# Optimization experiments

Measured on AMD Instinct MI355X. Metric: run time of the kernel, lower is better.

## Reference

```python
import jax, jax.numpy as jnp
import numpy as np

N_NODES, N_EDGES = 50000, 800000
IN_X, OUT_X = 32, 64
IN_EN, OUT_EN = 32, 64
HIDDEN = [64, 128, 32]  # build_mlp hidden sizes


def _mlp_params(key, dims):
    ps = []
    for i, (a, b) in enumerate(zip(dims[:-1], dims[1:])):
        k1, k2, key = jax.random.split(key, 3)
        s = 1.0 / np.sqrt(a)
        ps.append(jax.random.uniform(k1, (a, b), jnp.float32, -s, s))
        ps.append(jax.random.uniform(k2, (b,), jnp.float32, -s, s))
    return ps


def _mlp_apply(h, params):
    n_layers = len(params) // 2
    for i in range(n_layers):
        W, b = params[2 * i], params[2 * i + 1]
        h = h @ W + b
        if i < n_layers - 1:
            h = jax.nn.relu(h)
    return h


def setup_inputs() -> dict:
    key = jax.random.key(0)
    kx, ken, ks, kd, kt, kp, k_ten, k_pen = jax.random.split(key, 8)
    inp = {
        "x": jax.random.normal(kx, (N_NODES, IN_X), jnp.float32),
        "en": jax.random.normal(ken, (N_NODES, IN_EN), jnp.float32),
        "src": jax.random.randint(ks, (N_EDGES,), 0, N_NODES),
        "dst": jax.random.randint(kd, (N_EDGES,), 0, N_NODES),
    }
    # linear layers theta/phi for x
    kt1, kt2 = jax.random.split(kt)
    kp1, kp2 = jax.random.split(kp)
    s = 1.0 / np.sqrt(IN_X)
    inp["theta_W"] = jax.random.uniform(kt1, (IN_X, OUT_X), jnp.float32, -s, s)
    inp["theta_b"] = jax.random.uniform(kt2, (OUT_X,), jnp.float32, -s, s)
    inp["phi_W"] = jax.random.uniform(kp1, (IN_X, OUT_X), jnp.float32, -s, s)
    inp["phi_b"] = jax.random.uniform(kp2, (OUT_X,), jnp.float32, -s, s)
    # MLPs theta_en / phi_en: in_en -> 64 -> 128 -> 32 -> out_en
    dims = [IN_EN] + HIDDEN + [OUT_EN]
    for name, p in zip(
        ["ten_W0", "ten_b0", "ten_W1", "ten_b1", "ten_W2", "ten_b2", "ten_W3", "ten_b3"],
        _mlp_params(k_ten, dims)):
        inp[name] = p
    for name, p in zip(
        ["pen_W0", "pen_b0", "pen_W1", "pen_b1", "pen_W2", "pen_b2", "pen_W3", "pen_b3"],
        _mlp_params(k_pen, dims)):
        inp[name] = p
    return inp


def reference(x, en, src, dst,
              theta_W, theta_b, phi_W, phi_b,
              ten_W0, ten_b0, ten_W1, ten_b1, ten_W2, ten_b2, ten_W3, ten_b3,
              pen_W0, pen_b0, pen_W1, pen_b1, pen_W2, pen_b2, pen_W3, pen_b3):
    n = x.shape[0]
    ten = [ten_W0, ten_b0, ten_W1, ten_b1, ten_W2, ten_b2, ten_W3, ten_b3]
    pen = [pen_W0, pen_b0, pen_W1, pen_b1, pen_W2, pen_b2, pen_W3, pen_b3]

    # --- message: per-edge features ---
    dx = x[dst] - x[src]                       # [E, in_x]
    edge_x = dx @ theta_W + theta_b + (x @ phi_W + phi_b)[src]   # [E, out_x]
    den = en[dst] - en[src]                    # [E, in_en]
    edge_en = _mlp_apply(den, ten) + _mlp_apply(en, pen)[src]    # [E, out_en]

    # --- aggregate: max over incoming edge_x, mean over incoming edge_en ---
    deg = jax.ops.segment_sum(jnp.ones((src.shape[0],), x.dtype), dst, num_segments=n)
    has_in = (deg > 0)[:, None]
    x_new = jax.ops.segment_max(edge_x, dst, num_segments=n)
    x_new = jnp.where(has_in, x_new, 0.0)      # DGL zero-fills empty nodes
    en_sum = jax.ops.segment_sum(edge_en, dst, num_segments=n)
    en_new = en_sum / jnp.maximum(deg, 1.0)[:, None]

    # knn_graph rebuild is a library call (excluded from the kernel target);
    # return the updated node features carried by the new graph.
    return jnp.concatenate([x_new, en_new], axis=-1)  # [N, out_x + out_en]
```

## Files before the change

### kernel.cpp

```cpp
#include <hip/hip_runtime.h>

#define N_NODES 50000
#define N_EDGES 800000

typedef __attribute__((ext_vector_type(8))) short short8v;
typedef __attribute__((ext_vector_type(4))) float f32x4;

__device__ __forceinline__ ushort bf16hi(float v) {
  return (ushort)(__float_as_uint(v) >> 16);
}

__device__ __forceinline__ void split8(const float v[8], short8v& hh, short8v& ll) {
#pragma unroll
  for (int j = 0; j < 8; ++j) {
    unsigned uv = __float_as_uint(v[j]);
    hh[j] = (short)(uv >> 16);
    float hf = __uint_as_float(uv & 0xFFFF0000u);
    ll[j] = (short)(__float_as_uint(v[j] - hf) >> 16);
  }
}

#define C1_X 196
#define C1_CNT 3125
#define C1_PACK 120

constexpr int XK_THT = 0;
constexpr int XK_PHT = 2048;
constexpr int XK_THB = 4096;
constexpr int XK_PHB = 4160;
constexpr int XK_SZ  = 4224;

__global__ void __launch_bounds__(256) combo1_kernel(
    const float* __restrict__ x,
    const float* __restrict__ thW, const float* __restrict__ thB,
    const float* __restrict__ phW, const float* __restrict__ phB,
    float* __restrict__ out, float* __restrict__ gp,
    const int* __restrict__ dst, int* __restrict__ counts,
    const float* __restrict__ tW1, const float* __restrict__ tW2,
    const float* __restrict__ tW0, const float* __restrict__ pW0,
    const float* __restrict__ pW1, const float* __restrict__ pW2,
    const float* __restrict__ pW3, ushort* __restrict__ wp) {
  const int b = blockIdx.x;
  const int tid = threadIdx.x;
  if (b < C1_X) {
    __shared__ __align__(16) float sm[XK_SZ];
    for (int t = tid; t < 2048; t += 256) {
      int j = t >> 5, k = t & 31;
      sm[XK_THT + t] = thW[k * 64 + j];
      sm[XK_PHT + t] = phW[k * 64 + j];
    }
    for (int t = tid; t < 64; t += 256) {
      sm[XK_THB + t] = thB[t];
      sm[XK_PHB + t] = phB[t];
    }
    __syncthreads();
    int n = b * 256 + tid;
    if (n >= N_NODES) return;

    float xv[32];
    {
      const float4* p = (const float4*)(x + (long)n * 32);
#pragma unroll
      for (int q = 0; q < 8; ++q) {
        float4 v = p[q];
        xv[q * 4 + 0] = v.x; xv[q * 4 + 1] = v.y;
        xv[q * 4 + 2] = v.z; xv[q * 4 + 3] = v.w;
      }
    }
    float* ao = out + (long)n * 128;
    float* go = gp + (long)n * 128;
    for (int j = 0; j < 64; ++j) {
      float dth = 0.f, dph = 0.f;
#pragma unroll
      for (int k = 0; k < 32; ++k) {
        dth += xv[k] * sm[XK_THT + j * 32 + k];
        dph += xv[k] * sm[XK_PHT + j * 32 + k];
      }
      ao[j] = sm[XK_THB + j] + dth;
      go[j] = sm[XK_PHB + j] + dph - dth;
    }
  } else if (b < C1_X + C1_CNT) {
    int e = (b - C1_X) * 256 + tid;
    if (e < N_EDGES) atomicAdd(&counts[dst[e]], 1);
  } else {
    int t = (b - C1_X - C1_CNT) * 256 + tid;
    if (t >= 30720) return;
    float v;
    int hi_off, lo_off;
    if (t < 8192) {
      int fi = t >> 9, lane = (t >> 3) & 63, j = t & 7;
      int r = fi >> 1, f = fi & 1;
      int k2 = r * 16 + (lane & 15);
      int jg = f * 32 + (lane >> 4) * 8 + j;
      v = tW1[jg * 128 + k2];
      hi_off = t; lo_off = 8192 + t;
    } else if (t < 12288) {
      int t2 = t - 8192;
      int fi = t2 >> 9, lane = (t2 >> 3) & 63, j = t2 & 7;
      int tt = fi >> 2, f2 = fi & 3;
      int cc = tt * 16 + (lane & 15);
      int qq = (lane >> 4) & 3;
      int k2 = f2 * 32 + (j >> 2) * 16 + qq * 4 + (j & 3);
      v = tW2[k2 * 32 + cc];
      hi_off = 16384 + t2; lo_off = 20480 + t2;
    } else if (t < 16384) {
      int t3 = t - 12288;
      const float* M = (t3 < 2048) ? tW0 : pW0;
      int tt3 = t3 & 2047;
      int fi = tt3 >> 9, lane = (tt3 >> 3) & 63, j = tt3 & 7;
      int row = fi * 16 + (lane & 15);
      int k = (lane >> 4) * 8 + j;
      v = M[k * 64 + row];
      hi_off = ((t3 < 2048) ? 24576 : 28672) + tt3;
      lo_off = hi_off + 2048;
    } else if (t < 24576) {
      int t5 = t - 16384;
      int fi = t5 >> 9, lane = (t5 >> 3) & 63, j = t5 & 7;
      int r = fi >> 1, f = fi & 1;
      int row = r * 16 + (lane & 15);
      int sig = 32 * f + 16 * (j >> 2) + 4 * ((lane >> 4) & 3) + (j & 3);
      v = pW1[sig * 128 + row];
      hi_off = 32768 + t5; lo_off = 40960 + t5;
    } else if (t < 28672) {
      int t6 = t - 24576;
      int fi = t6 >> 9, lane = (t6 >> 3) & 63, j = t6 & 7;
      int tt = fi >> 2, f2 = fi & 3;
      int cc = tt * 16 + (lane & 15);
      int qq = (lane >> 4) & 3;
      int k2 = f2 * 32 + (j >> 2) * 16 + qq * 4 + (j & 3);
      v = pW2[k2 * 32 + cc];
      hi_off = 49152 + t6; lo_off = 53248 + t6;
    } else {
      int t7 = t - 28672;
      int fi = t7 >> 9, lane = (t7 >> 3) & 63, j = t7 & 7;
      int row = fi * 16 + (lane & 15);
      int sig = 16 * (j >> 2) + 4 * ((lane >> 4) & 3) + (j & 3);
      v = pW3[sig * 64 + row];
      hi_off = 57344 + t7; lo_off = 59392 + t7;
    }
    ushort h = bf16hi(v);
    float hf = __uint_as_float((unsigned)h << 16);
    ushort l = bf16hi(v - hf);
    wp[hi_off] = h;
    wp[lo_off] = l;
  }
}

#define SCAN_NB ((N_NODES + 1023) / 1024)

__global__ void __launch_bounds__(1024) scan1_kernel(
    const int* __restrict__ counts, int* __restrict__ offsets,
    int* __restrict__ bsum) {
  __shared__ int wsum[16];
  int t = threadIdx.x, b = blockIdx.x;
  int idx = b * 1024 + t;
  int c = (idx < N_NODES) ? counts[idx] : 0;
  int lane = t & 63, w = t >> 6;
  int v = c;
#pragma unroll
  for (int off = 1; off < 64; off <<= 1) {
    int tt = __shfl_up(v, off);
    if (lane >= off) v += tt;
  }
  if (lane == 63) wsum[w] = v;
  __syncthreads();
  int wpre = 0;
#pragma unroll
  for (int i = 0; i < 16; ++i) {
    int tt = wsum[i];
    if (i < w) wpre += tt;
  }
  int incl = v + wpre;
  if (idx < N_NODES) offsets[idx] = incl - c;
  if (t == 1023) bsum[b] = incl;
}

__global__ void __launch_bounds__(1024) scan2_kernel(
    const int* __restrict__ bsum, int* __restrict__ offsets,
    int* __restrict__ counts) {
  __shared__ int sb[SCAN_NB];
  int t = threadIdx.x, b = blockIdx.x;
  if (t < SCAN_NB) sb[t] = bsum[t];
  __syncthreads();
  int bpre = 0;
#pragma unroll
  for (int i = 0; i < SCAN_NB; ++i) {
    int tt = sb[i];
    if (i < b) bpre += tt;
  }
  int idx = b * 1024 + t;
  if (idx < N_NODES) {
    int v = offsets[idx] + bpre;
    offsets[idx] = v;
    counts[idx] = v;
  }
  if (b == 0 && t == 0) offsets[N_NODES] = N_EDGES;
}

#define C2_EN 391
#define C2_SC 1563

__global__ void __launch_bounds__(512) combo2_kernel(
    const float* __restrict__ en, const ushort* __restrict__ wp,
    const float* __restrict__ pb0, const float* __restrict__ pb1,
    const float* __restrict__ pb2, const float* __restrict__ pb3,
    float* __restrict__ u, float* __restrict__ gp,
    const int* __restrict__ src, const int* __restrict__ dst,
    int* __restrict__ cursor, int2* __restrict__ csr) {
  const int b = blockIdx.x;
  const int tid = threadIdx.x;
  if (b < C2_EN) {
    __shared__ __align__(16) ushort lds[36864];
    {
      const uint4* s4 = (const uint4*)(wp + 24576);
      uint4* d4 = (uint4*)lds;
      for (int i = tid; i < 4608; i += 512) d4[i] = s4[i];
    }
    __syncthreads();
    const int lane = tid & 63, q = lane >> 4, c = lane & 15, wv = tid >> 6;
    const int n = (b * 8 + wv) * 16 + c;
    const bool valid = n < N_NODES;

    float env[8];
#pragma unroll
    for (int j = 0; j < 8; ++j) env[j] = 0.f;
    if (valid) {
      const float4* p = (const float4*)(en + (long)n * 32 + q * 8);
      float4 e0 = p[0], e1 = p[1];
      env[0] = e0.x; env[1] = e0.y; env[2] = e0.z; env[3] = e0.w;
      env[4] = e1.x; env[5] = e1.y; env[6] = e1.z; env[7] = e1.w;
    }
    short8v beh, bel;
    split8(env, beh, bel);

    const short8v* TW0H = (const short8v*)(lds);
    const short8v* TW0L = (const short8v*)(lds + 2048);
    const short8v* PW0H = (const short8v*)(lds + 4096);
    const short8v* PW0L = (const short8v*)(lds + 6144);
    const short8v* NW1H = (const short8v*)(lds + 8192);
    const short8v* NW1L = (const short8v*)(lds + 16384);
    const short8v* NW2H = (const short8v*)(lds + 24576);
    const short8v* NW2L = (const short8v*)(lds + 28672);
    const short8v* NW3H = (const short8v*)(lds + 32768);
    const short8v* NW3L = (const short8v*)(lds + 34816);

#pragma unroll
    for (int t = 0; t < 4; ++t) {
      f32x4 a = {0.f, 0.f, 0.f, 0.f};
      short8v ah = TW0H[t * 64 + lane], al = TW0L[t * 64 + lane];
      a = __builtin_amdgcn_mfma_f32_16x16x32_bf16(ah, beh, a, 0, 0, 0);
      a = __builtin_amdgcn_mfma_f32_16x16x32_bf16(al, beh, a, 0, 0, 0);
      a = __builtin_amdgcn_mfma_f32_16x16x32_bf16(ah, bel, a, 0, 0, 0);
      if (valid) *(f32x4*)(u + (long)n * 64 + t * 16 + q * 4) = a;
    }

    float h0v[4][4];
#pragma unroll
    for (int t = 0; t < 4; ++t) {
      f32x4 a = *(const f32x4*)(pb0 + t * 16 + q * 4);
      short8v ah = PW0H[t * 64 + lane], al = PW0L[t * 64 + lane];
      a = __builtin_amdgcn_mfma_f32_16x16x32_bf16(ah, beh, a, 0, 0, 0);
      a = __builtin_amdgcn_mfma_f32_16x16x32_bf16(al, beh, a, 0, 0, 0);
      a = __builtin_amdgcn_mfma_f32_16x16x32_bf16(ah, bel, a, 0, 0, 0);
#pragma unroll
      for (int g = 0; g < 4; ++g) h0v[t][g] = fmaxf(a[g], 0.f);
    }

    short8v b1h[2], b1l[2];
#pragma unroll
    for (int f = 0; f < 2; ++f) {
      float tmp[8];
#pragma unroll
      for (int j = 0; j < 8; ++j) tmp[j] = h0v[2 * f + (j >> 2)][j & 3];
      split8(tmp, b1h[f], b1l[f]);
    }

    float h1v[8][4];
#pragma unroll
    for (int r = 0; r < 8; ++r) {
      f32x4 a = *(const f32x4*)(pb1 + r * 16 + q * 4);
#pragma unroll
      for (int f = 0; f < 2; ++f) {
        short8v ah = NW1H[(r * 2 + f) * 64 + lane];
        short8v al = NW1L[(r * 2 + f) * 64 + lane];
        a = __builtin_amdgcn_mfma_f32_16x16x32_bf16(ah, b1h[f], a, 0, 0, 0);
        a = __builtin_amdgcn_mfma_f32_16x16x32_bf16(al, b1h[f], a, 0, 0, 0);
        a = __builtin_amdgcn_mfma_f32_16x16x32_bf16(ah, b1l[f], a, 0, 0, 0);
      }
#pragma unroll
      for (int g = 0; g < 4; ++g) h1v[r][g] = fmaxf(a[g], 0.f);
    }

    short8v b2h[4], b2l[4];
#pragma unroll
    for (int f2 = 0; f2 < 4; ++f2) {
      float tmp[8];
#pragma unroll
      for (int j = 0; j < 8; ++j) tmp[j] = h1v[2 * f2 + (j >> 2)][j & 3];
      split8(tmp, b2h[f2], b2l[f2]);
    }

    float h2v[2][4];
#pragma unroll
    for (int tt = 0; tt < 2; ++tt) {
      f32x4 a = *(const f32x4*)(pb2 + tt * 16 + q * 4);
#pragma unroll
      for (int f2 = 0; f2 < 4; ++f2) {
        short8v ah = NW2H[(tt * 4 + f2) * 64 + lane];
        short8v al = NW2L[(tt * 4 + f2) * 64 + lane];
        a = __builtin_amdgcn_mfma_f32_16x16x32_bf16(ah, b2h[f2], a, 0, 0, 0);
        a = __builtin_amdgcn_mfma_f32_16x16x32_bf16(al, b2h[f2], a, 0, 0, 0);
        a = __builtin_amdgcn_mfma_f32_16x16x32_bf16(ah, b2l[f2], a, 0, 0, 0);
      }
#pragma unroll
      for (int g = 0; g < 4; ++g) h2v[tt][g] = fmaxf(a[g], 0.f);
    }

    short8v b3h, b3l;
    {
      float tmp[8];
#pragma unroll
      for (int j = 0; j < 8; ++j) tmp[j] = h2v[j >> 2][j & 3];
      split8(tmp, b3h, b3l);
    }

#pragma unroll
    for (int t = 0; t < 4; ++t) {
      f32x4 a = *(const f32x4*)(pb3 + t * 16 + q * 4);
      short8v ah = NW3H[t * 64 + lane], al = NW3L[t * 64 + lane];
      a = __builtin_amdgcn_mfma_f32_16x16x32_bf16(ah, b3h, a, 0, 0, 0);
      a = __builtin_amdgcn_mfma_f32_16x16x32_bf16(al, b3h, a, 0, 0, 0);
      a = __builtin_amdgcn_mfma_f32_16x16x32_bf16(ah, b3l, a, 0, 0, 0);
      if (valid) *(f32x4*)(gp + (long)n * 128 + 64 + t * 16 + q * 4) = a;
    }
  } else {
    int e = (b - C2_EN) * 512 + tid;
    if (e >= N_EDGES) return;
    int d = dst[e];
    int slot = atomicAdd(&cursor[d], 1);
    csr[slot] = make_int2(src[e], d);
  }
}

__global__ void __launch_bounds__(512) mlp_edge_kernel(
    const float* __restrict__ u,
    const int2* __restrict__ csr,
    const float* __restrict__ b0g, const float* __restrict__ b1g,
    const float* __restrict__ b2g,
    const ushort* __restrict__ wp,
    float* __restrict__ h2sum) {
  __shared__ __align__(16) ushort lds[24576];
  {
    const uint4* s4 = (const uint4*)wp;
    uint4* d4 = (uint4*)lds;
    for (int i = threadIdx.x; i < 3072; i += 512) d4[i] = s4[i];
  }
  __syncthreads();

  const int orig = blockIdx.x;
  const int xcd = orig & 7, loc = orig >> 3;
  const int blk = (xcd < 2) ? xcd * 782 + loc
                            : 2 * 782 + (xcd - 2) * 781 + loc;

  const int lane = threadIdx.x & 63;
  const int q = lane >> 4, c = lane & 15;
  const int wv = threadIdx.x >> 6;
  const int e = (blk * 8 + wv) * 16 + c;
  const int2 pr = csr[e];
  const int s = pr.x, d = pr.y;

  const short8v* W1HI = (const short8v*)(lds);
  const short8v* W1LO = (const short8v*)(lds + 8192);
  const short8v* W2HI = (const short8v*)(lds + 16384);
  const short8v* W2LO = (const short8v*)(lds + 20480);

  short8v bh0, bl0, bh1, bl1;
  {
    const float* ud = u + (long)d * 64 + q * 8;
    const float* us = u + (long)s * 64 + q * 8;
    const float* bp = b0g + q * 8;
#pragma unroll
    for (int f = 0; f < 2; ++f) {
      float4 d0 = *(const float4*)(ud + f * 32);
      float4 d1 = *(const float4*)(ud + f * 32 + 4);
      float4 s0 = *(const float4*)(us + f * 32);
      float4 s1 = *(const float4*)(us + f * 32 + 4);
      float4 c0 = *(const float4*)(bp + f * 32);
      float4 c1 = *(const float4*)(bp + f * 32 + 4);
      float v[8];
      v[0] = fmaxf(d0.x - s0.x + c0.x, 0.f);
      v[1] = fmaxf(d0.y - s0.y + c0.y, 0.f);
      v[2] = fmaxf(d0.z - s0.z + c0.z, 0.f);
      v[3] = fmaxf(d0.w - s0.w + c0.w, 0.f);
      v[4] = fmaxf(d1.x - s1.x + c1.x, 0.f);
      v[5] = fmaxf(d1.y - s1.y + c1.y, 0.f);
      v[6] = fmaxf(d1.z - s1.z + c1.z, 0.f);
      v[7] = fmaxf(d1.w - s1.w + c1.w, 0.f);
      short8v hh, ll;
      split8(v, hh, ll);
      if (f == 0) { bh0 = hh; bl0 = ll; } else { bh1 = hh; bl1 = ll; }
    }
  }

  f32x4 acc[8];
#pragma unroll
  for (int r = 0; r < 8; ++r)
    acc[r] = *(const f32x4*)(b1g + r * 16 + q * 4);
#pragma unroll
  for (int r = 0; r < 8; ++r) {
    short8v ah0 = W1HI[(2 * r) * 64 + lane];
    short8v ah1 = W1HI[(2 * r + 1) * 64 + lane];
    short8v al0 = W1LO[(2 * r) * 64 + lane];
    short8v al1 = W1LO[(2 * r + 1) * 64 + lane];
    acc[r] = __builtin_amdgcn_mfma_f32_16x16x32_bf16(ah0, bh0, acc[r], 0, 0, 0);
    acc[r] = __builtin_amdgcn_mfma_f32_16x16x32_bf16(ah1, bh1, acc[r], 0, 0, 0);
    acc[r] = __builtin_amdgcn_mfma_f32_16x16x32_bf16(al0, bh0, acc[r], 0, 0, 0);
    acc[r] = __builtin_amdgcn_mfma_f32_16x16x32_bf16(al1, bh1, acc[r], 0, 0, 0);
    acc[r] = __builtin_amdgcn_mfma_f32_16x16x32_bf16(ah0, bl0, acc[r], 0, 0, 0);
    acc[r] = __builtin_amdgcn_mfma_f32_16x16x32_bf16(ah1, bl1, acc[r], 0, 0, 0);
  }
  float h1v[8][4];
#pragma unroll
  for (int r = 0; r < 8; ++r)
#pragma unroll
    for (int g = 0; g < 4; ++g) h1v[r][g] = fmaxf(acc[r][g], 0.f);

  short8v b2h[4], b2l[4];
#pragma unroll
  for (int f2 = 0; f2 < 4; ++f2) {
    float tmp[8];
#pragma unroll
    for (int j = 0; j < 8; ++j) tmp[j] = h1v[2 * f2 + (j >> 2)][j & 3];
    split8(tmp, b2h[f2], b2l[f2]);
  }

  f32x4 a20 = *(const f32x4*)(b2g + q * 4);
  f32x4 a21 = *(const f32x4*)(b2g + 16 + q * 4);
#pragma unroll
  for (int f2 = 0; f2 < 4; ++f2) {
    short8v ah = W2HI[f2 * 64 + lane];
    short8v al = W2LO[f2 * 64 + lane];
    a20 = __builtin_amdgcn_mfma_f32_16x16x32_bf16(ah, b2h[f2], a20, 0, 0, 0);
    a20 = __builtin_amdgcn_mfma_f32_16x16x32_bf16(al, b2h[f2], a20, 0, 0, 0);
    a20 = __builtin_amdgcn_mfma_f32_16x16x32_bf16(ah, b2l[f2], a20, 0, 0, 0);
    short8v ah1 = W2HI[(4 + f2) * 64 + lane];
    short8v al1 = W2LO[(4 + f2) * 64 + lane];
    a21 = __builtin_amdgcn_mfma_f32_16x16x32_bf16(ah1, b2h[f2], a21, 0, 0, 0);
    a21 = __builtin_amdgcn_mfma_f32_16x16x32_bf16(al1, b2h[f2], a21, 0, 0, 0);
    a21 = __builtin_amdgcn_mfma_f32_16x16x32_bf16(ah1, b2l[f2], a21, 0, 0, 0);
  }
  float h2v[8];
#pragma unroll
  for (int g = 0; g < 4; ++g) {
    h2v[g] = fmaxf(a20[g], 0.f);
    h2v[4 + g] = fmaxf(a21[g], 0.f);
  }

  int dp = __shfl_up(d, 1, 16);
  bool head = (c == 0) || (dp != d);
  int seg = head ? c : 0;
#pragma unroll
  for (int off = 1; off < 16; off <<= 1) {
    int t = __shfl_up(seg, off, 16);
    if (c >= off) seg = max(seg, t);
  }
#pragma unroll
  for (int off = 1; off < 16; off <<= 1) {
    bool take = (c - off) >= seg;
#pragma unroll
    for (int k = 0; k < 8; ++k) {
      float t = __shfl_up(h2v[k], off, 16);
      if (take) h2v[k] += t;
    }
  }
  int dn = __shfl_down(d, 1, 16);
  bool tail = (c == 15) || (dn != d);
  if (tail) {
    float* hs = h2sum + (long)d * 32 + q * 4;
#pragma unroll
    for (int g = 0; g < 4; ++g) atomicAdd(&hs[g], h2v[g]);
#pragma unroll
    for (int g = 0; g < 4; ++g) atomicAdd(&hs[16 + g], h2v[4 + g]);
  }
}

__global__ void __launch_bounds__(256) gather_kernel(
    const int2* __restrict__ csr, const int* __restrict__ offsets,
    const float* __restrict__ gp, const float* __restrict__ h2sum,
    const float* __restrict__ tW3, const float* __restrict__ tb3,
    float* __restrict__ out) {
  __shared__ float sW3[2048 + 64];
  for (int t = threadIdx.x; t < 2048; t += 256) sW3[t] = tW3[t];
  for (int t = threadIdx.x; t < 64; t += 256) sW3[2048 + t] = tb3[t];
  __syncthreads();
  int n = blockIdx.x * 8 + (threadIdx.x >> 5);
  int l = threadIdx.x & 31;
  int half = l >> 4, j4 = l & 15;
  int off = half * 64 + j4 * 4;
  int o0 = offsets[n], o1 = offsets[n + 1];
  int deg = o1 - o0;

  const float NEG = -3.402823466e38f;
  float4 mx = make_float4(NEG, NEG, NEG, NEG);
  float4 sm4 = make_float4(0.f, 0.f, 0.f, 0.f);
  for (int t = o0; t < o1; ++t) {
    int s = csr[t].x;
    float4 v = *(const float4*)(gp + (long)s * 128 + off);
    mx.x = fmaxf(mx.x, v.x); mx.y = fmaxf(mx.y, v.y);
    mx.z = fmaxf(mx.z, v.z); mx.w = fmaxf(mx.w, v.w);
    sm4.x += v.x; sm4.y += v.y; sm4.z += v.z; sm4.w += v.w;
  }

  float4 r;
  if (half == 0) {
    float4 a = *(const float4*)(out + (long)n * 128 + off);
    bool has = deg > 0;
    r.x = has ? a.x + mx.x : 0.f;
    r.y = has ? a.y + mx.y : 0.f;
    r.z = has ? a.z + mx.z : 0.f;
    r.w = has ? a.w + mx.w : 0.f;
  } else {
    int jj = j4 * 4;
    float w30 = 0.f, w31 = 0.f, w32 = 0.f, w33 = 0.f;
    const float* h2r = h2sum + (long)n * 32;
#pragma unroll
    for (int k = 0; k < 32; ++k) {
      float h = h2r[k];
      const float* wrow = &sW3[k * 64 + jj];
      w30 += h * wrow[0]; w31 += h * wrow[1];
      w32 += h * wrow[2]; w33 += h * wrow[3];
    }
    float dg = (float)deg;
    float inv = 1.f / fmaxf(dg, 1.f);
    r.x = (sm4.x + w30 + dg * sW3[2048 + jj + 0]) * inv;
    r.y = (sm4.y + w31 + dg * sW3[2048 + jj + 1]) * inv;
    r.z = (sm4.z + w32 + dg * sW3[2048 + jj + 2]) * inv;
    r.w = (sm4.w + w33 + dg * sW3[2048 + jj + 3]) * inv;
  }
  *(float4*)(out + (long)n * 128 + off) = r;
}

extern "C" void kernel_launch(void* const* d_in, const int* in_sizes, int n_in,
                              void* d_out, int out_size, void* d_ws,
                              size_t ws_size, hipStream_t stream) {
  const float* x   = (const float*)d_in[0];
  const float* en  = (const float*)d_in[1];
  const int* src   = (const int*)d_in[2];
  const int* dst   = (const int*)d_in[3];
  const float* thW = (const float*)d_in[4];
  const float* thB = (const float*)d_in[5];
  const float* phW = (const float*)d_in[6];
  const float* phB = (const float*)d_in[7];
  const float* tW0 = (const float*)d_in[8];
  const float* tb0 = (const float*)d_in[9];
  const float* tW1 = (const float*)d_in[10];
  const float* tb1 = (const float*)d_in[11];
  const float* tW2 = (const float*)d_in[12];
  const float* tb2 = (const float*)d_in[13];
  const float* tW3 = (const float*)d_in[14];
  const float* tb3 = (const float*)d_in[15];
  const float* pW0 = (const float*)d_in[16];
  const float* pb0 = (const float*)d_in[17];
  const float* pW1 = (const float*)d_in[18];
  const float* pb1 = (const float*)d_in[19];
  const float* pW2 = (const float*)d_in[20];
  const float* pb2 = (const float*)d_in[21];
  const float* pW3 = (const float*)d_in[22];
  const float* pb3 = (const float*)d_in[23];

  float* out = (float*)d_out;
  float* ws  = (float*)d_ws;
  float* gp     = ws;
  float* u      = ws + (long)N_NODES * 128;
  float* h2sum  = ws + (long)N_NODES * 192;
  float* wpf    = ws + (long)N_NODES * 224;
  ushort* wp    = (ushort*)wpf;
  int* iw       = (int*)(wpf + 30720);
  int2* csr     = (int2*)iw;
  int* counts   = iw + 2 * N_EDGES;
  int* offsets  = counts + N_NODES;
  int* bsum     = offsets + N_NODES + 1;

  hipMemsetAsync(counts, 0, N_NODES * sizeof(int), stream);
  hipMemsetAsync(h2sum, 0, (size_t)N_NODES * 32 * sizeof(float), stream);
  combo1_kernel<<<C1_X + C1_CNT + C1_PACK, 256, 0, stream>>>(
      x, thW, thB, phW, phB, out, gp, dst, counts,
      tW1, tW2, tW0, pW0, pW1, pW2, pW3, wp);
  scan1_kernel<<<SCAN_NB, 1024, 0, stream>>>(counts, offsets, bsum);
  scan2_kernel<<<SCAN_NB, 1024, 0, stream>>>(bsum, offsets, counts);
  combo2_kernel<<<C2_EN + C2_SC, 512, 0, stream>>>(
      en, wp, pb0, pb1, pb2, pb3, u, gp, src, dst, counts, csr);
  mlp_edge_kernel<<<N_EDGES / 128, 512, 0, stream>>>(
      u, csr, tb0, tb1, tb2, wp, h2sum);
  gather_kernel<<<N_NODES / 8, 256, 0, stream>>>(
      csr, offsets, gp, h2sum, tW3, tb3, out);
}
```

Baseline: 316.7 us.

## Run neighbor gather concurrently with edge MLP and split out finalize kernel

Moves the max/sum gather over the CSR neighbors into extra blocks of the edge MLP kernel, so the memory-bound gather runs alongside the MFMA-heavy edge MLP instead of after it. A lightweight finalize kernel then applies the W3 projection to h2sum, adds the bias and the partial sum stored in out, and normalizes by degree. The extra kernel launch and the round trip of the partial sum through out are the added cost. Gather blocks also allocate the 48KB LDS array even though they do not use it, which can limit how many of them are resident at once.

```diff
diff --git a/kernel.cpp b/kernel.cpp
--- a/kernel.cpp
+++ b/kernel.cpp
@@ -342,14 +342,53 @@
   }
 }
 
-__global__ void __launch_bounds__(512) mlp_edge_kernel(
+#define ME_EDGE 6250
+#define ME_GATH 3125
+
+__global__ void __launch_bounds__(512) edge_gather_kernel(
     const float* __restrict__ u,
     const int2* __restrict__ csr,
     const float* __restrict__ b0g, const float* __restrict__ b1g,
     const float* __restrict__ b2g,
     const ushort* __restrict__ wp,
-    float* __restrict__ h2sum) {
+    float* __restrict__ h2sum,
+    const int* __restrict__ offsets,
+    const float* __restrict__ gp, float* __restrict__ out) {
   __shared__ __align__(16) ushort lds[24576];
+  if (blockIdx.x >= ME_EDGE) {
+    int g = blockIdx.x - ME_EDGE;
+    int n = g * 16 + (threadIdx.x >> 5);
+    int l = threadIdx.x & 31;
+    int half = l >> 4, j4 = l & 15;
+    int off = half * 64 + j4 * 4;
+    int o0 = offsets[n], o1 = offsets[n + 1];
+    int deg = o1 - o0;
+
+    const float NEG = -3.402823466e38f;
+    float4 mx = make_float4(NEG, NEG, NEG, NEG);
+    float4 sm4 = make_float4(0.f, 0.f, 0.f, 0.f);
+    for (int t = o0; t < o1; ++t) {
+      int s = csr[t].x;
+      float4 v = *(const float4*)(gp + (long)s * 128 + off);
+      mx.x = fmaxf(mx.x, v.x); mx.y = fmaxf(mx.y, v.y);
+      mx.z = fmaxf(mx.z, v.z); mx.w = fmaxf(mx.w, v.w);
+      sm4.x += v.x; sm4.y += v.y; sm4.z += v.z; sm4.w += v.w;
+    }
+    float4 r;
+    if (half == 0) {
+      float4 a = *(const float4*)(out + (long)n * 128 + off);
+      bool has = deg > 0;
+      r.x = has ? a.x + mx.x : 0.f;
+      r.y = has ? a.y + mx.y : 0.f;
+      r.z = has ? a.z + mx.z : 0.f;
+      r.w = has ? a.w + mx.w : 0.f;
+    } else {
+      r = sm4;
+    }
+    *(float4*)(out + (long)n * 128 + off) = r;
+    return;
+  }
+
   {
     const uint4* s4 = (const uint4*)wp;
     uint4* d4 = (uint4*)lds;
@@ -484,60 +523,39 @@
   }
 }
 
-__global__ void __launch_bounds__(256) gather_kernel(
-    const int2* __restrict__ csr, const int* __restrict__ offsets,
-    const float* __restrict__ gp, const float* __restrict__ h2sum,
+__global__ void __launch_bounds__(256) finalize_kernel(
+    const int* __restrict__ offsets, const float* __restrict__ h2sum,
     const float* __restrict__ tW3, const float* __restrict__ tb3,
     float* __restrict__ out) {
   __shared__ float sW3[2048 + 64];
   for (int t = threadIdx.x; t < 2048; t += 256) sW3[t] = tW3[t];
   for (int t = threadIdx.x; t < 64; t += 256) sW3[2048 + t] = tb3[t];
   __syncthreads();
-  int n = blockIdx.x * 8 + (threadIdx.x >> 5);
-  int l = threadIdx.x & 31;
-  int half = l >> 4, j4 = l & 15;
-  int off = half * 64 + j4 * 4;
-  int o0 = offsets[n], o1 = offsets[n + 1];
-  int deg = o1 - o0;
-
-  const float NEG = -3.402823466e38f;
-  float4 mx = make_float4(NEG, NEG, NEG, NEG);
-  float4 sm4 = make_float4(0.f, 0.f, 0.f, 0.f);
-  for (int t = o0; t < o1; ++t) {
-    int s = csr[t].x;
-    float4 v = *(const float4*)(gp + (long)s * 128 + off);
-    mx.x = fmaxf(mx.x, v.x); mx.y = fmaxf(mx.y, v.y);
-    mx.z = fmaxf(mx.z, v.z); mx.w = fmaxf(mx.w, v.w);
-    sm4.x += v.x; sm4.y += v.y; sm4.z += v.z; sm4.w += v.w;
-  }
-
+  int n = blockIdx.x * 16 + (threadIdx.x >> 4);
+  int j4 = threadIdx.x & 15;
+  int jj = j4 * 4;
+  int deg = offsets[n + 1] - offsets[n];
+
+  float* po = out + (long)n * 128 + 64 + jj;
+  float4 ssum = *(const float4*)po;
+
+  float w30 = 0.f, w31 = 0.f, w32 = 0.f, w33 = 0.f;
+  const float* h2r = h2sum + (long)n * 32;
+#pragma unroll
+  for (int k = 0; k < 32; ++k) {
+    float h = h2r[k];
+    const float* wrow = &sW3[k * 64 + jj];
+    w30 += h * wrow[0]; w31 += h * wrow[1];
+    w32 += h * wrow[2]; w33 += h * wrow[3];
+  }
+  float dg = (float)deg;
+  float inv = 1.f / fmaxf(dg, 1.f);
   float4 r;
-  if (half == 0) {
-    float4 a = *(const float4*)(out + (long)n * 128 + off);
-    bool has = deg > 0;
-    r.x = has ? a.x + mx.x : 0.f;
-    r.y = has ? a.y + mx.y : 0.f;
-    r.z = has ? a.z + mx.z : 0.f;
-    r.w = has ? a.w + mx.w : 0.f;
-  } else {
-    int jj = j4 * 4;
-    float w30 = 0.f, w31 = 0.f, w32 = 0.f, w33 = 0.f;
-    const float* h2r = h2sum + (long)n * 32;
-#pragma unroll
-    for (int k = 0; k < 32; ++k) {
-      float h = h2r[k];
-      const float* wrow = &sW3[k * 64 + jj];
-      w30 += h * wrow[0]; w31 += h * wrow[1];
-      w32 += h * wrow[2]; w33 += h * wrow[3];
-    }
-    float dg = (float)deg;
-    float inv = 1.f / fmaxf(dg, 1.f);
-    r.x = (sm4.x + w30 + dg * sW3[2048 + jj + 0]) * inv;
-    r.y = (sm4.y + w31 + dg * sW3[2048 + jj + 1]) * inv;
-    r.z = (sm4.z + w32 + dg * sW3[2048 + jj + 2]) * inv;
-    r.w = (sm4.w + w33 + dg * sW3[2048 + jj + 3]) * inv;
-  }
-  *(float4*)(out + (long)n * 128 + off) = r;
+  r.x = (ssum.x + w30 + dg * sW3[2048 + jj + 0]) * inv;
+  r.y = (ssum.y + w31 + dg * sW3[2048 + jj + 1]) * inv;
+  r.z = (ssum.z + w32 + dg * sW3[2048 + jj + 2]) * inv;
+  r.w = (ssum.w + w33 + dg * sW3[2048 + jj + 3]) * inv;
+  *(float4*)po = r;
 }
 
 extern "C" void kernel_launch(void* const* d_in, const int* in_sizes, int n_in,
@@ -590,8 +608,8 @@
   scan2_kernel<<<SCAN_NB, 1024, 0, stream>>>(bsum, offsets, counts);
   combo2_kernel<<<C2_EN + C2_SC, 512, 0, stream>>>(
       en, wp, pb0, pb1, pb2, pb3, u, gp, src, dst, counts, csr);
-  mlp_edge_kernel<<<N_EDGES / 128, 512, 0, stream>>>(
-      u, csr, tb0, tb1, tb2, wp, h2sum);
-  gather_kernel<<<N_NODES / 8, 256, 0, stream>>>(
-      csr, offsets, gp, h2sum, tW3, tb3, out);
-}
+  edge_gather_kernel<<<ME_EDGE + ME_GATH, 512, 0, stream>>>(
+      u, csr, tb0, tb1, tb2, wp, h2sum, offsets, gp, out);
+  finalize_kernel<<<N_NODES / 16, 256, 0, stream>>>(
+      offsets, h2sum, tW3, tb3, out);
+}
```

Result: slower. 325.7 us (+2.8%).
